# Kernel tuning notes

Hardware: AMD Instinct MI355X
Metric: run time of the kernel (lower is better)

## Reference

```python
import itertools
import jax, jax.numpy as jnp
import numpy as np

EPS = 1e-15
B, K, H, W = 64, 8, 128, 128


def setup_inputs() -> dict:
    key = jax.random.key(0)
    k1, k2 = jax.random.split(key)
    pred_masks = jax.random.uniform(k1, (B, K, H, W), dtype=jnp.float32)
    aug_masks = jax.random.uniform(k2, (B, K, H, W), dtype=jnp.float32)
    return {"pred_masks": pred_masks, "aug_masks": aug_masks}


def _mask_kl_div(pred, true):
    # true * (log(true+eps) - log(pred+eps)), mean over (H, W)
    return (true * (jnp.log(true + EPS) - jnp.log(pred + EPS))).mean(axis=(-2, -1))


# all K! permutations, precomputed once (K=8 -> 40320 perms)
_PERMS = jnp.asarray(np.array(list(itertools.permutations(range(K))), dtype=np.int32))


def reference(pred_masks, aug_masks):
    b, k, h, w = pred_masks.shape
    t = aug_masks  # targets are detached in torch for the cost matrix
    # Fused pairwise KL cost matrix (avoids the (B,K,K,H,W) broadcast):
    # C[b,i,j] = mean_hw[ t_j*log(t_j+eps) ] - mean_hw[ t_j*log(p_i+eps) ]
    ent = (t * jnp.log(t + EPS)).mean(axis=(-2, -1))          # (B, K) over j
    cross = jnp.einsum('bjhw,bihw->bij', t, jnp.log(pred_masks + EPS)) / (h * w)
    C = ent[:, None, :] - cross                                # (B, K, K)
    # exact linear assignment via exhaustive search over K! permutations
    rows = jnp.arange(k)
    costs = C[:, rows[None, :], _PERMS].sum(axis=-1)           # (B, K!)
    R2C = _PERMS[jnp.argmin(costs, axis=1)]                    # (B, K) col for each row
    # permute rows: out[b, i] = pred[b, argsort(R2C)[b, i]]
    row_perm = jnp.argsort(R2C, axis=1)
    pred_perm = jnp.take_along_axis(pred_masks, row_perm[:, :, None, None], axis=1)
    l = _mask_kl_div(pred_perm, t)                             # (B, K)
    return l.mean(), pred_perm[..., None]
```

## Files before the change

### kernel.cpp

```cpp
#include <hip/hip_runtime.h>


#define BB 64
#define KK 8
#define HW 16384
#define SPANS 16
#define SPAN 1024
#define EPSF 1e-15f

struct MaskTab {
    unsigned char masks[255];
    int off[9];
};

constexpr MaskTab make_tab() {
    MaskTab t{};
    int idx = 0;
    for (int p = 1; p <= 8; ++p) {
        t.off[p - 1] = idx;
        for (int m = 1; m < 256; ++m) {
            int c = 0;
            for (int b = 0; b < 8; ++b) c += (m >> b) & 1;
            if (c == p) t.masks[idx++] = (unsigned char)m;
        }
    }
    t.off[8] = idx;
    return t;
}

__constant__ MaskTab kTab = make_tab();

__device__ __forceinline__ float dot4(float4 t, float4 l) {
    return t.x * l.x + t.y * l.y + t.z * l.z + t.w * l.w;
}

__device__ __forceinline__ float4 log4(float4 a) {
    float4 r;
    r.x = __logf(a.x + EPSF); r.y = __logf(a.y + EPSF);
    r.z = __logf(a.z + EPSF); r.w = __logf(a.w + EPSF);
    return r;
}

__global__ __launch_bounds__(256) void cost_kernel(const float* __restrict__ pred,
                                                   const float* __restrict__ aug,
                                                   float* __restrict__ part,
                                                   float* __restrict__ out)
{
    __shared__ float red[4][72];

    const int blk  = blockIdx.x;
    const int b    = blk >> 4;
    const int s    = blk & 15;
    const int tid  = threadIdx.x;
    const int wave = tid >> 6;
    const int lane = tid & 63;

    if (blk == 0 && tid == 0) out[0] = 0.f;

    const size_t base = (size_t)b * (KK * HW) + (size_t)s * SPAN + (size_t)tid * 4;
    const float* pp = pred + base;
    const float* ap = aug  + base;

    float4 pv[8], av[8];
#pragma unroll
    for (int i = 0; i < 8; ++i) pv[i] = *(const float4*)(pp + (size_t)i * HW);
#pragma unroll
    for (int j = 0; j < 8; ++j) av[j] = *(const float4*)(ap + (size_t)j * HW);
    __builtin_amdgcn_sched_barrier(0);

    float4 lp[8];
#pragma unroll
    for (int i = 0; i < 8; ++i) lp[i] = log4(pv[i]);

    float acc[64];
    float ent[8];
#pragma unroll
    for (int j = 0; j < 8; ++j) {
        const float4 a = av[j];
        ent[j] = dot4(a, log4(a));
#pragma unroll
        for (int i = 0; i < 8; ++i)
            acc[i * 8 + j] = dot4(a, lp[i]);
    }

#pragma unroll
    for (int r = 0; r < 6; ++r) {
        const int d    = 1 << r;
        const int half = 32 >> r;
        const bool hi  = (lane & d) != 0;
#pragma unroll
        for (int k = 0; k < half; ++k) {
            const float send = hi ? acc[k] : acc[k + half];
            const float recv = __shfl_xor(send, d);
            acc[k] = (hi ? acc[k + half] : acc[k]) + recv;
        }
    }

#pragma unroll
    for (int r = 0; r < 3; ++r) {
        const int d    = 1 << r;
        const int half = 4 >> r;
        const bool hi  = (lane & d) != 0;
#pragma unroll
        for (int k = 0; k < half; ++k) {
            const float send = hi ? ent[k] : ent[k + half];
            const float recv = __shfl_xor(send, d);
            ent[k] = (hi ? ent[k + half] : ent[k]) + recv;
        }
    }
    float ev = ent[0];
    ev += __shfl_xor(ev, 8);
    ev += __shfl_xor(ev, 16);
    ev += __shfl_xor(ev, 32);

    const int vidx = ((lane & 1) << 5) | ((lane & 2) << 3) | ((lane & 4) << 1) |
                     ((lane & 8) >> 1) | ((lane & 16) >> 3) | ((lane & 32) >> 5);
    red[wave][vidx] = acc[0];
    if (lane < 8)
        red[wave][64 + (((lane & 1) << 2) | (lane & 2) | ((lane & 4) >> 2))] = ev;
    __syncthreads();

    if (tid < 72) {
        const float ssum = red[0][tid] + red[1][tid] + red[2][tid] + red[3][tid];
        part[(size_t)blk * 72 + tid] = ssum;
    }
}

__global__ __launch_bounds__(256) void permute_kernel(const float* __restrict__ pred,
                                                      const float* __restrict__ part,
                                                      float* __restrict__ out)
{
    __shared__ float red[72];
    __shared__ float C[64];
    __shared__ float dp[256];
    __shared__ int   choice[256];
    __shared__ int   inv8[8];

    const int p    = blockIdx.x;
    const int b    = p >> 3;
    const int tid  = threadIdx.x;

    const float* pb = part + (size_t)b * SPANS * 72;
    if (tid < 72) {
        float s = 0.f;
#pragma unroll
        for (int c = 0; c < SPANS; ++c) s += pb[c * 72 + tid];
        red[tid] = s;
    }
    if (tid == 0) dp[0] = 0.f;
    __syncthreads();
    if (tid < 64) C[tid] = red[64 + (tid & 7)] - red[tid];
    __syncthreads();

    const int grp = tid >> 3;
    const int j   = tid & 7;
    for (int lvl = 1; lvl <= 8; ++lvl) {
        const int start = kTab.off[lvl - 1];
        const int end   = kTab.off[lvl];
        const float* Crow = &C[(lvl - 1) * 8];
        for (int bse = start; bse < end; bse += 32) {
            const int mi = bse + grp;
            if (mi < end) {
                const int M = kTab.masks[mi];
                float v  = 1e30f;
                int   bj = 0;
                if (M & (1 << j)) {
                    v  = dp[M ^ (1 << j)] + Crow[j];
                    bj = j;
                }
#pragma unroll
                for (int d = 1; d < 8; d <<= 1) {
                    const float ov = __shfl_xor(v, d);
                    const int   oj = __shfl_xor(bj, d);
                    if (ov < v) { v = ov; bj = oj; }
                }
                if (j == 0) { dp[M] = v; choice[M] = bj; }
            }
        }
        __syncthreads();
    }

    if (tid == 0) {
        int mask = 255;
        for (int r = 7; r >= 0; --r) {
            const int jj = choice[mask];
            inv8[jj] = r;
            mask ^= 1 << jj;
        }
        if ((p & 7) == 0)
            atomicAdd(out, dp[255] * (1.0f / (16384.0f * 512.0f)));
    }
    __syncthreads();

    const int src_row = inv8[p & 7];
    const float* src  = pred + ((size_t)(b << 3) + src_row) * HW;
    float*      drow  = out + 1 + (size_t)p * HW;

#pragma unroll
    for (int m = 0; m < 16; ++m) {
        const int f = tid + 256 * m;
        const int e = 3 + 4 * f;
        if (f < 4095) {
            float4 v;
            v.x = src[e]; v.y = src[e + 1]; v.z = src[e + 2]; v.w = src[e + 3];
            *(float4*)(drow + e) = v;
        } else {
            drow[0] = src[0]; drow[1] = src[1]; drow[2] = src[2];
            drow[16383] = src[16383];
        }
    }
}

extern "C" void kernel_launch(void* const* d_in, const int* in_sizes, int n_in,
                              void* d_out, int out_size, void* d_ws, size_t ws_size,
                              hipStream_t stream) {
    const float* pred = (const float*)d_in[0];
    const float* aug  = (const float*)d_in[1];
    float* out = (float*)d_out;
    float* part = (float*)d_ws;

    cost_kernel<<<dim3(BB * SPANS), dim3(256), 0, stream>>>(pred, aug, part, out);
    permute_kernel<<<dim3(512), dim3(256), 0, stream>>>(pred, part, out);
}
```

Baseline: 120.6 us.

## Repartition cost kernel per (batch,row) block with full-row loop over aug rows

The cost kernel now assigns each block one pred row of one batch and loops over the whole spatial extent, accumulating dot products against all 8 aug rows, instead of splitting space into 16 spans that each compute the full 8x8 partial matrix. This cuts per-thread accumulators from 64 to 8 and shrinks the shuffle reduction and partial-sum storage. The permute kernel then reads the 9 values per block directly, with no span summation. In exchange, each aug row is read by 8 different blocks, which raises global and cache traffic, and the entropy term is computed inside the loop under a row check.

Result: no change. 121.6 us (+0.8%).

```diff
diff --git a/kernel.cpp b/kernel.cpp
--- a/kernel.cpp
+++ b/kernel.cpp
@@ -4,8 +4,6 @@
 #define BB 64
 #define KK 8
 #define HW 16384
-#define SPANS 16
-#define SPAN 1024
 #define EPSF 1e-15f
 
 struct MaskTab {
@@ -46,47 +44,46 @@
                                                    float* __restrict__ part,
                                                    float* __restrict__ out)
 {
-    __shared__ float red[4][72];
-
-    const int blk  = blockIdx.x;
-    const int b    = blk >> 4;
-    const int s    = blk & 15;
+    __shared__ float red[4][9];
+
+    const int p    = blockIdx.x;
+    const int i    = p >> 6;
+    const int b    = p & 63;
     const int tid  = threadIdx.x;
     const int wave = tid >> 6;
     const int lane = tid & 63;
 
-    if (blk == 0 && tid == 0) out[0] = 0.f;
-
-    const size_t base = (size_t)b * (KK * HW) + (size_t)s * SPAN + (size_t)tid * 4;
-    const float* pp = pred + base;
-    const float* ap = aug  + base;
-
-    float4 pv[8], av[8];
-#pragma unroll
-    for (int i = 0; i < 8; ++i) pv[i] = *(const float4*)(pp + (size_t)i * HW);
-#pragma unroll
-    for (int j = 0; j < 8; ++j) av[j] = *(const float4*)(ap + (size_t)j * HW);
-    __builtin_amdgcn_sched_barrier(0);
-
-    float4 lp[8];
-#pragma unroll
-    for (int i = 0; i < 8; ++i) lp[i] = log4(pv[i]);
-
-    float acc[64];
-    float ent[8];
-#pragma unroll
-    for (int j = 0; j < 8; ++j) {
-        const float4 a = av[j];
-        ent[j] = dot4(a, log4(a));
-#pragma unroll
-        for (int i = 0; i < 8; ++i)
-            acc[i * 8 + j] = dot4(a, lp[i]);
-    }
-
-#pragma unroll
-    for (int r = 0; r < 6; ++r) {
+    if (p == 0 && tid == 0) out[0] = 0.f;
+
+    const float* prow  = pred + ((size_t)b * KK + i) * HW;
+    const float* abase = aug  + (size_t)b * KK * HW;
+
+    float acc[8];
+#pragma unroll
+    for (int j = 0; j < 8; ++j) acc[j] = 0.f;
+    float eacc = 0.f;
+
+    const int rot = p & 15;
+
+    for (int m = 0; m < 16; ++m) {
+        const int mm = (m + rot) & 15;
+        const int e  = (tid + 256 * mm) * 4;
+
+        const float4 pq = *(const float4*)(prow + e);
+        const float4 la = log4(pq);
+
+#pragma unroll
+        for (int j = 0; j < 8; ++j) {
+            const float4 a = *(const float4*)(abase + (size_t)j * HW + e);
+            acc[j] += dot4(a, la);
+            if (j == i) eacc += dot4(a, log4(a));
+        }
+    }
+
+#pragma unroll
+    for (int r = 0; r < 3; ++r) {
         const int d    = 1 << r;
-        const int half = 32 >> r;
+        const int half = 4 >> r;
         const bool hi  = (lane & d) != 0;
 #pragma unroll
         for (int k = 0; k < half; ++k) {
@@ -95,42 +92,28 @@
             acc[k] = (hi ? acc[k + half] : acc[k]) + recv;
         }
     }
-
-#pragma unroll
-    for (int r = 0; r < 3; ++r) {
-        const int d    = 1 << r;
-        const int half = 4 >> r;
-        const bool hi  = (lane & d) != 0;
-#pragma unroll
-        for (int k = 0; k < half; ++k) {
-            const float send = hi ? ent[k] : ent[k + half];
-            const float recv = __shfl_xor(send, d);
-            ent[k] = (hi ? ent[k + half] : ent[k]) + recv;
-        }
-    }
-    float ev = ent[0];
-    ev += __shfl_xor(ev, 8);
-    ev += __shfl_xor(ev, 16);
-    ev += __shfl_xor(ev, 32);
-
-    const int vidx = ((lane & 1) << 5) | ((lane & 2) << 3) | ((lane & 4) << 1) |
-                     ((lane & 8) >> 1) | ((lane & 16) >> 3) | ((lane & 32) >> 5);
-    red[wave][vidx] = acc[0];
+    float av = acc[0];
+    av += __shfl_xor(av, 8);
+    av += __shfl_xor(av, 16);
+    av += __shfl_xor(av, 32);
+
+#pragma unroll
+    for (int d = 1; d < 64; d <<= 1) eacc += __shfl_xor(eacc, d);
+
     if (lane < 8)
-        red[wave][64 + (((lane & 1) << 2) | (lane & 2) | ((lane & 4) >> 2))] = ev;
+        red[wave][((lane & 1) << 2) | (lane & 2) | ((lane & 4) >> 2)] = av;
+    if (lane == 0)
+        red[wave][8] = eacc;
     __syncthreads();
 
-    if (tid < 72) {
-        const float ssum = red[0][tid] + red[1][tid] + red[2][tid] + red[3][tid];
-        part[(size_t)blk * 72 + tid] = ssum;
-    }
+    if (tid < 9)
+        part[(size_t)p * 9 + tid] = red[0][tid] + red[1][tid] + red[2][tid] + red[3][tid];
 }
 
 __global__ __launch_bounds__(256) void permute_kernel(const float* __restrict__ pred,
                                                       const float* __restrict__ part,
                                                       float* __restrict__ out)
 {
-    __shared__ float red[72];
     __shared__ float C[64];
     __shared__ float dp[256];
     __shared__ int   choice[256];
@@ -140,16 +123,13 @@
     const int b    = p >> 3;
     const int tid  = threadIdx.x;
 
-    const float* pb = part + (size_t)b * SPANS * 72;
-    if (tid < 72) {
-        float s = 0.f;
-#pragma unroll
-        for (int c = 0; c < SPANS; ++c) s += pb[c * 72 + tid];
-        red[tid] = s;
+    if (tid < 64) {
+        const int ii = tid >> 3, jj = tid & 7;
+        const float cross = part[((size_t)ii * 64 + b) * 9 + jj];
+        const float entj  = part[((size_t)jj * 64 + b) * 9 + 8];
+        C[tid] = entj - cross;
     }
     if (tid == 0) dp[0] = 0.f;
-    __syncthreads();
-    if (tid < 64) C[tid] = red[64 + (tid & 7)] - red[tid];
     __syncthreads();
 
     const int grp = tid >> 3;
@@ -216,9 +196,9 @@
                               hipStream_t stream) {
     const float* pred = (const float*)d_in[0];
     const float* aug  = (const float*)d_in[1];
-    float* out = (float*)d_out;
+    float* out  = (float*)d_out;
     float* part = (float*)d_ws;
 
-    cost_kernel<<<dim3(BB * SPANS), dim3(256), 0, stream>>>(pred, aug, part, out);
+    cost_kernel<<<dim3(512), dim3(256), 0, stream>>>(pred, aug, part, out);
     permute_kernel<<<dim3(512), dim3(256), 0, stream>>>(pred, part, out);
 }
```
